# Optimization experiments

Measured on AMD Instinct MI355X. Metric: run time of the kernel, lower is better.

Reference implementation:

```python
import jax, jax.numpy as jnp
import numpy as np

C = 256
NUM_HEADS = 4
GROUPS = 8
EPS = 1e-5


def setup_inputs() -> dict:
    key = jax.random.key(0)
    ks = jax.random.split(key, 7)
    B, H, W = 4, 64, 64
    x = jax.random.normal(ks[0], (B, C, H, W), dtype=jnp.float32)
    # GroupNorm affine params
    norm_w = jnp.ones((C,), dtype=jnp.float32)
    norm_b = jnp.zeros((C,), dtype=jnp.float32)
    # 1x1 convs == channel-mixing matrices
    qkv_w = jax.random.normal(ks[1], (3 * C, C), dtype=jnp.float32) * (C ** -0.5)
    qkv_b = jnp.zeros((3 * C,), dtype=jnp.float32)
    proj_w = jax.random.normal(ks[2], (C, C), dtype=jnp.float32) * (C ** -0.5)
    proj_b = jnp.zeros((C,), dtype=jnp.float32)
    return {"x": x, "norm_w": norm_w, "norm_b": norm_b,
            "qkv_w": qkv_w, "qkv_b": qkv_b,
            "proj_w": proj_w, "proj_b": proj_b}


def _group_norm(x, w, b):
    B, Cc, H, W = x.shape
    xr = x.reshape(B, GROUPS, Cc // GROUPS, H * W)
    mean = xr.mean(axis=(2, 3), keepdims=True)
    var = xr.var(axis=(2, 3), keepdims=True)
    xn = ((xr - mean) * jax.lax.rsqrt(var + EPS)).reshape(B, Cc, H, W)
    return xn * w[None, :, None, None] + b[None, :, None, None]


def reference(x, norm_w, norm_b, qkv_w, qkv_b, proj_w, proj_b):
    B, Cc, H, W = x.shape
    nh = NUM_HEADS
    d = Cc // nh
    h = _group_norm(x, norm_w, norm_b)
    # 1x1 conv: channel matmul
    qkv = jnp.einsum('oc,bchw->bohw', qkv_w, h) + qkv_b[None, :, None, None]
    q, k, v = jnp.split(qkv, 3, axis=1)
    q = q.reshape(B, nh, d, H * W)
    k = k.reshape(B, nh, d, H * W)
    v = v.reshape(B, nh, d, H * W)
    scale = d ** -0.5
    attn = jnp.einsum('bhci,bhcj->bhij', q, k) * scale  # [B, nh, HW, HW]
    attn = jax.nn.softmax(attn, axis=-1)
    o = jnp.einsum('bhij,bhcj->bhci', attn, v).reshape(B, Cc, H, W)
    out = jnp.einsum('oc,bchw->bohw', proj_w, o) + proj_b[None, :, None, None]
    return x + out
```

## Files before the change

kernel.cpp:

```cpp
#include <hip/hip_runtime.h>

typedef unsigned short u16;
typedef __attribute__((ext_vector_type(8))) short bf16x8;
typedef __attribute__((ext_vector_type(16))) float f32x16;
typedef __attribute__((ext_vector_type(2))) int i32x2;

#define MFMA32(A, B, C) __builtin_amdgcn_mfma_f32_32x32x16_bf16((A), (B), (C), 0, 0, 0)

#define BB 4
#define CC 256
#define HW 4096
#define NH 4
#define HD 64

#define QSCALE 0.18033688f

__device__ __forceinline__ u16 f2bf(float f) {
  unsigned int u = __builtin_bit_cast(unsigned int, f);
  u += 0x7fffu + ((u >> 16) & 1u);
  return (u16)(u >> 16);
}

__device__ __forceinline__ unsigned cvtpk(float a, float b) {
  unsigned r;
  asm("v_cvt_pk_bf16_f32 %0, %1, %2" : "=v"(r) : "v"(a), "v"(b));
  return r;
}

__device__ __forceinline__ uint4 pack_oct(const f32x16& a, int oct, float scl) {
  const int b8 = oct * 8;
  unsigned A0 = cvtpk(a[b8 + 0] * scl, a[b8 + 1] * scl);
  unsigned A1 = cvtpk(a[b8 + 2] * scl, a[b8 + 3] * scl);
  unsigned B0 = cvtpk(a[b8 + 4] * scl, a[b8 + 5] * scl);
  unsigned B1 = cvtpk(a[b8 + 6] * scl, a[b8 + 7] * scl);
  i32x2 r0 = __builtin_amdgcn_permlane32_swap((int)A0, (int)B0, false, false);
  i32x2 r1 = __builtin_amdgcn_permlane32_swap((int)A1, (int)B1, false, false);
  union { unsigned w[4]; uint4 v; } u;
  u.w[0] = (unsigned)r0[0]; u.w[1] = (unsigned)r1[0];
  u.w[2] = (unsigned)r0[1]; u.w[3] = (unsigned)r1[1];
  return u.v;
}

__global__ __launch_bounds__(256) void w2bf_kernel(const float* __restrict__ qw,
                                                   const float* __restrict__ pw,
                                                   u16* __restrict__ w_f) {
  int wv = (blockIdx.x * 256 + threadIdx.x) >> 6;
  int lane = threadIdx.x & 63;
  int row = (wv >> 4) * 32 + (lane & 31);
  int c0 = (wv & 15) * 16 + (lane >> 5) * 8;
  const float* src = (row < 768) ? (qw + (size_t)row * 256 + c0)
                                 : (pw + (size_t)(row - 768) * 256 + c0);
  float4 a = *(const float4*)src;
  float4 b = *(const float4*)(src + 4);
  union { u16 u[8]; uint4 v; } pk;
  pk.u[0] = f2bf(a.x); pk.u[1] = f2bf(a.y); pk.u[2] = f2bf(a.z); pk.u[3] = f2bf(a.w);
  pk.u[4] = f2bf(b.x); pk.u[5] = f2bf(b.y); pk.u[6] = f2bf(b.z); pk.u[7] = f2bf(b.w);
  *(uint4*)(w_f + ((size_t)wv * 64 + lane) * 8) = pk.v;
}

__global__ __launch_bounds__(256) void gn_partial_kernel(const float* __restrict__ x,
                                                         float* __restrict__ partial) {
  const float4* p = (const float4*)(x + (size_t)blockIdx.x * 16384);
  float s = 0.f, ss = 0.f;
  for (int i = threadIdx.x; i < 4096; i += 256) {
    float4 v = p[i];
    s += (v.x + v.y) + (v.z + v.w);
    ss += (v.x * v.x + v.y * v.y) + (v.z * v.z + v.w * v.w);
  }
#pragma unroll
  for (int msk = 32; msk; msk >>= 1) {
    s += __shfl_xor(s, msk);
    ss += __shfl_xor(ss, msk);
  }
  __shared__ float red[2][4];
  int wave = threadIdx.x >> 6;
  if ((threadIdx.x & 63) == 0) { red[0][wave] = s; red[1][wave] = ss; }
  __syncthreads();
  if (threadIdx.x == 0) {
    partial[blockIdx.x] = red[0][0] + red[0][1] + red[0][2] + red[0][3];
    partial[256 + blockIdx.x] = red[1][0] + red[1][1] + red[1][2] + red[1][3];
  }
}

__global__ __launch_bounds__(64) void gn_final_kernel(const float* __restrict__ partial,
                                                      float* __restrict__ stats) {
  int bg = threadIdx.x;
  if (bg < 32) {
    float S = 0.f, SS = 0.f;
#pragma unroll
    for (int sp = 0; sp < 8; ++sp) {
      S += partial[bg * 8 + sp];
      SS += partial[256 + bg * 8 + sp];
    }
    const float invN = 1.0f / 131072.0f;
    float mean = S * invN;
    float var = SS * invN - mean * mean;
    stats[bg] = mean;
    stats[32 + bg] = rsqrtf(var + 1e-5f);
  }
}

__global__ __launch_bounds__(256) void norm_t_kernel(const float* __restrict__ x,
                                                     const float* __restrict__ nw,
                                                     const float* __restrict__ nb,
                                                     const float* __restrict__ stats,
                                                     u16* __restrict__ h_f) {
  __shared__ u16 L[256][66];
  int b = blockIdx.y;
  int s0 = blockIdx.x * 64;
  int lane = threadIdx.x & 63, w = threadIdx.x >> 6;
  int c_off = lane >> 4;
  int s_off = (lane & 15) * 4;
  const float* xb = x + (size_t)b * CC * HW;
#pragma unroll 4
  for (int cc = 0; cc < 16; ++cc) {
    int c = w * 64 + cc * 4 + c_off;
    int g = c >> 5;
    float mean = stats[b * 8 + g];
    float rstd = stats[32 + b * 8 + g];
    float a = nw[c] * rstd;
    float b2 = nb[c] - mean * a;
    float4 v = *(const float4*)(xb + (size_t)c * HW + s0 + s_off);
    union { u16 u[4]; uint2 q; } pk;
    pk.u[0] = f2bf(v.x * a + b2);
    pk.u[1] = f2bf(v.y * a + b2);
    pk.u[2] = f2bf(v.z * a + b2);
    pk.u[3] = f2bf(v.w * a + b2);
    *(uint2*)&L[c][s_off] = pk.q;
  }
  __syncthreads();
  u16* hb = h_f + (size_t)b * HW * CC;
  int ql = lane & 31, hi = lane >> 5;
  for (int t = w; t < 32; t += 4) {
    int s32t = t >> 4, kc = t & 15;
    int c0 = kc * 16 + hi * 8;
    int s = s32t * 32 + ql;
    union { u16 u[8]; uint4 v; } pk;
#pragma unroll
    for (int j = 0; j < 8; ++j) pk.u[j] = L[c0 + j][s];
    int s32g = (s0 >> 5) + s32t;
    *(uint4*)(hb + ((size_t)(s32g * 16 + kc) * 64 + lane) * 8) = pk.v;
  }
}

__global__ __launch_bounds__(256) void qkv_kernel(const u16* __restrict__ h_f,
                                                  const u16* __restrict__ w_f,
                                                  const float* __restrict__ qb,
                                                  u16* __restrict__ q_f,
                                                  u16* __restrict__ k_f,
                                                  u16* __restrict__ v_f) {
  int b = blockIdx.z;
  int y = blockIdx.y;
  int lane = threadIdx.x & 63, wave = threadIdx.x >> 6;
  int ql = lane & 31, hi = lane >> 5;
  int s0w = blockIdx.x * 128 + (wave >> 1) * 64;
  int o0w = y * 128 + (wave & 1) * 64;
  bool isV = (y >= 4);
  const u16* hb = h_f + (size_t)b * HW * CC;

  f32x16 acc[2][2];
  if (!isV) {
#pragma unroll
    for (int mo = 0; mo < 2; ++mo)
#pragma unroll
      for (int r = 0; r < 16; ++r) {
        int row = (r & 3) + 8 * (r >> 2) + 4 * hi;
        float bv = qb[o0w + mo * 32 + row];
        acc[mo][0][r] = bv;
        acc[mo][1][r] = bv;
      }
  } else {
#pragma unroll
    for (int ns = 0; ns < 2; ++ns) {
      float bv = qb[o0w + ns * 32 + ql];
#pragma unroll
      for (int r = 0; r < 16; ++r) {
        acc[0][ns][r] = bv;
        acc[1][ns][r] = bv;
      }
    }
  }

  int os32 = o0w >> 5, ss32 = s0w >> 5;
  const u16* wp = w_f + ((size_t)(os32 * 16) * 64 + lane) * 8;
  const u16* hp = hb + ((size_t)(ss32 * 16) * 64 + lane) * 8;
  bf16x8 wf[2], hf[2], wn[2], hn[2];
  wf[0] = *(const bf16x8*)(wp);
  wf[1] = *(const bf16x8*)(wp + 16 * 512);
  hf[0] = *(const bf16x8*)(hp);
  hf[1] = *(const bf16x8*)(hp + 16 * 512);
#pragma unroll 1
  for (int kk = 0; kk < 16; ++kk) {
    if (kk < 15) {
      wn[0] = *(const bf16x8*)(wp + (size_t)(kk + 1) * 512);
      wn[1] = *(const bf16x8*)(wp + (size_t)(16 + kk + 1) * 512);
      hn[0] = *(const bf16x8*)(hp + (size_t)(kk + 1) * 512);
      hn[1] = *(const bf16x8*)(hp + (size_t)(16 + kk + 1) * 512);
    }
    if (!isV) {
      acc[0][0] = MFMA32(wf[0], hf[0], acc[0][0]);
      acc[0][1] = MFMA32(wf[0], hf[1], acc[0][1]);
      acc[1][0] = MFMA32(wf[1], hf[0], acc[1][0]);
      acc[1][1] = MFMA32(wf[1], hf[1], acc[1][1]);
    } else {
      acc[0][0] = MFMA32(hf[0], wf[0], acc[0][0]);
      acc[0][1] = MFMA32(hf[0], wf[1], acc[0][1]);
      acc[1][0] = MFMA32(hf[1], wf[0], acc[1][0]);
      acc[1][1] = MFMA32(hf[1], wf[1], acc[1][1]);
    }
    wf[0] = wn[0]; wf[1] = wn[1]; hf[0] = hn[0]; hf[1] = hn[1];
  }

  if (!isV) {
    bool isQ = (y < 2);
    float scl = isQ ? QSCALE : 1.0f;
    int headL = (o0w >> 6) - (isQ ? 0 : 4);
    u16* base = (isQ ? q_f : k_f) + (size_t)(b * NH + headL) * HW * HD;
#pragma unroll
    for (int mo = 0; mo < 2; ++mo)
#pragma unroll
      for (int ns = 0; ns < 2; ++ns) {
        int s32 = ss32 + ns;
#pragma unroll
        for (int oct = 0; oct < 2; ++oct) {
          int kc = mo * 2 + oct;
          uint4 v = pack_oct(acc[mo][ns], oct, scl);
          *(uint4*)(base + ((size_t)(s32 * 4 + kc) * 64 + lane) * 8) = v;
        }
      }
  } else {
    int headv = (o0w >> 6) - 8;
    u16* base = v_f + (size_t)(b * NH + headv) * HW * HD;
#pragma unroll
    for (int mo = 0; mo < 2; ++mo)
#pragma unroll
      for (int ns = 0; ns < 2; ++ns)
#pragma unroll
        for (int oct = 0; oct < 2; ++oct) {
          int kvb = s0w + mo * 32 + oct * 16;
          int jb64 = kvb >> 6, kcv = (kvb & 63) >> 4;
          uint4 v = pack_oct(acc[mo][ns], oct, 1.0f);
          *(uint4*)(base + ((size_t)((jb64 * 2 + ns) * 4 + kcv) * 64 + lane) * 8) = v;
        }
  }
}

__global__ __launch_bounds__(512) void attn_kernel(const u16* __restrict__ q_f,
                                                   const u16* __restrict__ k_f,
                                                   const u16* __restrict__ v_f,
                                                   u16* __restrict__ o_f) {
  __shared__ float mbuf[4 * 33 * 64];
  int wgid = blockIdx.x + gridDim.x * blockIdx.y;
  int xcd = wgid & 7;
  int j = wgid >> 3;
  int bh = (xcd << 1) | (j & 1);
  int qblk = j >> 1;
  int tid = threadIdx.x;
  int wave = tid >> 6, lane = tid & 63;
  int half = wave >> 2, wsub = wave & 3;
  int ql = lane & 31, hi = lane >> 5;
  int q0w = qblk * 128 + wsub * 32;
  const u16* qfb = q_f + (size_t)bh * HW * HD + lane * 8;
  const u16* kfb = k_f + (size_t)bh * HW * HD + lane * 8;
  const u16* vfb = v_f + (size_t)bh * HW * HD + lane * 8;

  int s32q = q0w >> 5;
  bf16x8 qf[4];
#pragma unroll
  for (int kc = 0; kc < 4; ++kc)
    qf[kc] = *(const bf16x8*)(qfb + (size_t)(s32q * 4 + kc) * 512);

  float l_run = 0.f;
  f32x16 of0 = {}, of1 = {};
  bf16x8 kfr[8], vfr[8];

  {
    const u16* kb = kfb + (size_t)half * 4096;
    const u16* vb = vfb + (size_t)half * 4096;
#pragma unroll
    for (int kc = 0; kc < 4; ++kc) {
      kfr[kc] = *(const bf16x8*)(kb + (size_t)kc * 512);
      kfr[4 + kc] = *(const bf16x8*)(kb + (size_t)(4 + kc) * 512);
      vfr[kc] = *(const bf16x8*)(vb + (size_t)kc * 512);
      vfr[4 + kc] = *(const bf16x8*)(vb + (size_t)(4 + kc) * 512);
    }
  }

#pragma unroll 1
  for (int it = half; it < 64; it += 2) {
    f32x16 s0 = {}, s1 = {};
    __builtin_amdgcn_s_setprio(1);
#pragma unroll
    for (int kc = 0; kc < 4; ++kc) {
      s0 = MFMA32(kfr[kc], qf[kc], s0);
      s1 = MFMA32(kfr[4 + kc], qf[kc], s1);
    }
    __builtin_amdgcn_s_setprio(0);

    {
      const u16* kb = kfb + (size_t)(it + 2) * 4096;
#pragma unroll
      for (int kc = 0; kc < 4; ++kc) {
        kfr[kc] = *(const bf16x8*)(kb + (size_t)kc * 512);
        kfr[4 + kc] = *(const bf16x8*)(kb + (size_t)(4 + kc) * 512);
      }
    }

#pragma unroll
    for (int i = 0; i < 16; ++i) {
      s0[i] = __builtin_amdgcn_exp2f(s0[i]);
      s1[i] = __builtin_amdgcn_exp2f(s1[i]);
    }

    bf16x8 pf[4];
#pragma unroll
    for (int kc = 0; kc < 4; ++kc) {
      const f32x16 pv = (kc < 2) ? s0 : s1;
      const int b8 = (kc & 1) * 8;
      unsigned A0 = cvtpk(pv[b8 + 0], pv[b8 + 1]);
      unsigned A1 = cvtpk(pv[b8 + 2], pv[b8 + 3]);
      unsigned B0 = cvtpk(pv[b8 + 4], pv[b8 + 5]);
      unsigned B1 = cvtpk(pv[b8 + 6], pv[b8 + 7]);
      i32x2 r0 = __builtin_amdgcn_permlane32_swap((int)A0, (int)B0, false, false);
      i32x2 r1 = __builtin_amdgcn_permlane32_swap((int)A1, (int)B1, false, false);
      union { unsigned w[4]; bf16x8 v8; } u;
      u.w[0] = (unsigned)r0[0]; u.w[1] = (unsigned)r1[0];
      u.w[2] = (unsigned)r0[1]; u.w[3] = (unsigned)r1[1];
      pf[kc] = u.v8;
    }

    __builtin_amdgcn_s_setprio(1);
#pragma unroll
    for (int kc = 0; kc < 4; ++kc) {
      of0 = MFMA32(vfr[kc], pf[kc], of0);
      of1 = MFMA32(vfr[4 + kc], pf[kc], of1);
    }
    __builtin_amdgcn_s_setprio(0);

    {
      const u16* vb = vfb + (size_t)(it + 2) * 4096;
#pragma unroll
      for (int kc = 0; kc < 4; ++kc) {
        vfr[kc] = *(const bf16x8*)(vb + (size_t)kc * 512);
        vfr[4 + kc] = *(const bf16x8*)(vb + (size_t)(4 + kc) * 512);
      }
    }

    float t8[8];
#pragma unroll
    for (int i = 0; i < 8; ++i)
      t8[i] = (s0[i] + s0[i + 8]) + (s1[i] + s1[i + 8]);
    float t4a = t8[0] + t8[4], t4b = t8[1] + t8[5];
    float t4c = t8[2] + t8[6], t4d = t8[3] + t8[7];
    l_run += (t4a + t4b) + (t4c + t4d);
  }

  __syncthreads();
  if (half == 1) {
    float* mb = mbuf + (size_t)wsub * 33 * 64 + lane;
#pragma unroll
    for (int i = 0; i < 16; ++i) mb[i * 64] = of0[i];
#pragma unroll
    for (int i = 0; i < 16; ++i) mb[(16 + i) * 64] = of1[i];
    mb[32 * 64] = l_run;
  }
  __syncthreads();
  if (half == 0) {
    const float* mb = mbuf + (size_t)wsub * 33 * 64 + lane;
#pragma unroll
    for (int i = 0; i < 16; ++i) of0[i] += mb[i * 64];
#pragma unroll
    for (int i = 0; i < 16; ++i) of1[i] += mb[(16 + i) * 64];
    l_run += mb[32 * 64];
    float l_tot = l_run + __shfl_xor(l_run, 32);
    float inv_l = 1.0f / l_tot;
    int bb = bh >> 2, hh = bh & 3;
    u16* obase = o_f + (size_t)bb * HW * CC;
    int q32 = q0w >> 5;
#pragma unroll
    for (int cb = 0; cb < 2; ++cb) {
      const f32x16 o = cb ? of1 : of0;
#pragma unroll
      for (int oct = 0; oct < 2; ++oct) {
        int ck = hh * 4 + cb * 2 + oct;
        uint4 v = pack_oct(o, oct, inv_l);
        *(uint4*)(obase + ((size_t)(q32 * 16 + ck) * 64 + lane) * 8) = v;
      }
    }
  }
}

__global__ __launch_bounds__(256) void proj_kernel(const u16* __restrict__ o_f,
                                                   const u16* __restrict__ w_f,
                                                   const float* __restrict__ pb,
                                                   const float* __restrict__ x,
                                                   float* __restrict__ out) {
  int b = blockIdx.z;
  int lane = threadIdx.x & 63, wave = threadIdx.x >> 6;
  int ql = lane & 31, hi = lane >> 5;
  int s0w = blockIdx.x * 128 + (wave >> 1) * 64;
  int o0w = blockIdx.y * 128 + (wave & 1) * 64;
  const u16* ob = o_f + (size_t)b * HW * CC;

  f32x16 acc[2][2];
#pragma unroll
  for (int mo = 0; mo < 2; ++mo)
#pragma unroll
    for (int r = 0; r < 16; ++r) {
      int row = (r & 3) + 8 * (r >> 2) + 4 * hi;
      float bv = pb[o0w + mo * 32 + row];
      acc[mo][0][r] = bv;
      acc[mo][1][r] = bv;
    }

  int os32 = 24 + (o0w >> 5), ss32 = s0w >> 5;
  const u16* wp = w_f + ((size_t)(os32 * 16) * 64 + lane) * 8;
  const u16* op2 = ob + ((size_t)(ss32 * 16) * 64 + lane) * 8;
  bf16x8 af[2], bf2[2], an[2], bn[2];
  af[0] = *(const bf16x8*)(wp);
  af[1] = *(const bf16x8*)(wp + 16 * 512);
  bf2[0] = *(const bf16x8*)(op2);
  bf2[1] = *(const bf16x8*)(op2 + 16 * 512);
#pragma unroll 1
  for (int kk = 0; kk < 16; ++kk) {
    if (kk < 15) {
      an[0] = *(const bf16x8*)(wp + (size_t)(kk + 1) * 512);
      an[1] = *(const bf16x8*)(wp + (size_t)(16 + kk + 1) * 512);
      bn[0] = *(const bf16x8*)(op2 + (size_t)(kk + 1) * 512);
      bn[1] = *(const bf16x8*)(op2 + (size_t)(16 + kk + 1) * 512);
    }
    acc[0][0] = MFMA32(af[0], bf2[0], acc[0][0]);
    acc[0][1] = MFMA32(af[0], bf2[1], acc[0][1]);
    acc[1][0] = MFMA32(af[1], bf2[0], acc[1][0]);
    acc[1][1] = MFMA32(af[1], bf2[1], acc[1][1]);
    af[0] = an[0]; af[1] = an[1]; bf2[0] = bn[0]; bf2[1] = bn[1];
  }

#pragma unroll
  for (int mo = 0; mo < 2; ++mo)
#pragma unroll
    for (int r = 0; r < 16; ++r) {
      int o = o0w + mo * 32 + (r & 3) + 8 * (r >> 2) + 4 * hi;
      const float* xp = x + ((size_t)b * CC + o) * HW + s0w + ql;
      float* op = out + ((size_t)b * CC + o) * HW + s0w + ql;
      op[0] = acc[mo][0][r] + xp[0];
      op[32] = acc[mo][1][r] + xp[32];
    }
}

extern "C" void kernel_launch(void* const* d_in, const int* in_sizes, int n_in,
                              void* d_out, int out_size, void* d_ws, size_t ws_size,
                              hipStream_t stream) {
  const float* x = (const float*)d_in[0];
  const float* nw = (const float*)d_in[1];
  const float* nb = (const float*)d_in[2];
  const float* qw = (const float*)d_in[3];
  const float* qb = (const float*)d_in[4];
  const float* pw = (const float*)d_in[5];
  const float* pb = (const float*)d_in[6];
  float* out = (float*)d_out;

  float* stats = (float*)d_ws;
  float* partial = stats + 64;
  u16* h_f = (u16*)((char*)d_ws + 4096);
  u16* q_f = h_f + (size_t)BB * HW * CC;
  u16* k_f = q_f + (size_t)BB * HW * CC;
  u16* v_f = k_f + (size_t)BB * HW * CC;
  u16* w_f = v_f + (size_t)BB * HW * CC;
  u16* o_f = h_f;

  gn_partial_kernel<<<256, 256, 0, stream>>>(x, partial);
  gn_final_kernel<<<1, 64, 0, stream>>>(partial, stats);
  w2bf_kernel<<<128, 256, 0, stream>>>(qw, pw, w_f);
  norm_t_kernel<<<dim3(HW / 64, BB), 256, 0, stream>>>(x, nw, nb, stats, h_f);
  qkv_kernel<<<dim3(HW / 128, 6, BB), 256, 0, stream>>>(h_f, w_f, qb, q_f, k_f, v_f);
  attn_kernel<<<dim3(HW / 128, BB * NH), 512, 0, stream>>>(q_f, k_f, v_f, o_f);
  proj_kernel<<<dim3(HW / 128, 2, BB), 256, 0, stream>>>(o_f, w_f, pb, x, out);
}
```

Before: 138.1 us.

## Stage h tile in LDS and loop all six output blocks per workgroup in qkv

The qkv kernel now loads the 128-position activation tile once into shared memory and loops over all six 128-row output-channel blocks inside one workgroup, instead of launching one workgroup per output block. This removes the sixfold re-read of h from global memory. In exchange the grid shrinks sixfold (128 workgroups), the register double-buffering prefetch of weights is dropped, and weight loads now sit directly before the MFMAs with no overlap.

```diff
diff --git a/kernel.cpp b/kernel.cpp
--- a/kernel.cpp
+++ b/kernel.cpp
@@ -149,99 +149,106 @@
                                                   u16* __restrict__ q_f,
                                                   u16* __restrict__ k_f,
                                                   u16* __restrict__ v_f) {
-  int b = blockIdx.z;
-  int y = blockIdx.y;
+  __shared__ __align__(16) u16 hL[4][16][64 * 8];
+  int b = blockIdx.y;
   int lane = threadIdx.x & 63, wave = threadIdx.x >> 6;
   int ql = lane & 31, hi = lane >> 5;
-  int s0w = blockIdx.x * 128 + (wave >> 1) * 64;
-  int o0w = y * 128 + (wave & 1) * 64;
-  bool isV = (y >= 4);
+  int s0 = blockIdx.x * 128;
+  int ss32 = s0 >> 5;
   const u16* hb = h_f + (size_t)b * HW * CC;
 
-  f32x16 acc[2][2];
-  if (!isV) {
-#pragma unroll
-    for (int mo = 0; mo < 2; ++mo)
-#pragma unroll
-      for (int r = 0; r < 16; ++r) {
-        int row = (r & 3) + 8 * (r >> 2) + 4 * hi;
-        float bv = qb[o0w + mo * 32 + row];
-        acc[mo][0][r] = bv;
-        acc[mo][1][r] = bv;
-      }
-  } else {
-#pragma unroll
-    for (int ns = 0; ns < 2; ++ns) {
-      float bv = qb[o0w + ns * 32 + ql];
-#pragma unroll
-      for (int r = 0; r < 16; ++r) {
-        acc[0][ns][r] = bv;
-        acc[1][ns][r] = bv;
-      }
-    }
-  }
-
-  int os32 = o0w >> 5, ss32 = s0w >> 5;
-  const u16* wp = w_f + ((size_t)(os32 * 16) * 64 + lane) * 8;
-  const u16* hp = hb + ((size_t)(ss32 * 16) * 64 + lane) * 8;
-  bf16x8 wf[2], hf[2], wn[2], hn[2];
-  wf[0] = *(const bf16x8*)(wp);
-  wf[1] = *(const bf16x8*)(wp + 16 * 512);
-  hf[0] = *(const bf16x8*)(hp);
-  hf[1] = *(const bf16x8*)(hp + 16 * 512);
+  {
+    const u16* src = hb + ((size_t)((ss32 + wave) * 16) * 64 + lane) * 8;
+#pragma unroll
+    for (int kc = 0; kc < 16; ++kc)
+      *(uint4*)&hL[wave][kc][lane * 8] = *(const uint4*)(src + (size_t)kc * 512);
+  }
+  __syncthreads();
+
+  int sw = wave >> 1;
+  int ow = wave & 1;
 #pragma unroll 1
-  for (int kk = 0; kk < 16; ++kk) {
-    if (kk < 15) {
-      wn[0] = *(const bf16x8*)(wp + (size_t)(kk + 1) * 512);
-      wn[1] = *(const bf16x8*)(wp + (size_t)(16 + kk + 1) * 512);
-      hn[0] = *(const bf16x8*)(hp + (size_t)(kk + 1) * 512);
-      hn[1] = *(const bf16x8*)(hp + (size_t)(16 + kk + 1) * 512);
-    }
+  for (int y = 0; y < 6; ++y) {
+    int o0w = y * 128 + ow * 64;
+    bool isV = (y >= 4);
+    f32x16 acc[2][2];
     if (!isV) {
-      acc[0][0] = MFMA32(wf[0], hf[0], acc[0][0]);
-      acc[0][1] = MFMA32(wf[0], hf[1], acc[0][1]);
-      acc[1][0] = MFMA32(wf[1], hf[0], acc[1][0]);
-      acc[1][1] = MFMA32(wf[1], hf[1], acc[1][1]);
+#pragma unroll
+      for (int mo = 0; mo < 2; ++mo)
+#pragma unroll
+        for (int r = 0; r < 16; ++r) {
+          int row = (r & 3) + 8 * (r >> 2) + 4 * hi;
+          float bv = qb[o0w + mo * 32 + row];
+          acc[mo][0][r] = bv;
+          acc[mo][1][r] = bv;
+        }
     } else {
-      acc[0][0] = MFMA32(hf[0], wf[0], acc[0][0]);
-      acc[0][1] = MFMA32(hf[0], wf[1], acc[0][1]);
-      acc[1][0] = MFMA32(hf[1], wf[0], acc[1][0]);
-      acc[1][1] = MFMA32(hf[1], wf[1], acc[1][1]);
-    }
-    wf[0] = wn[0]; wf[1] = wn[1]; hf[0] = hn[0]; hf[1] = hn[1];
-  }
-
-  if (!isV) {
-    bool isQ = (y < 2);
-    float scl = isQ ? QSCALE : 1.0f;
-    int headL = (o0w >> 6) - (isQ ? 0 : 4);
-    u16* base = (isQ ? q_f : k_f) + (size_t)(b * NH + headL) * HW * HD;
-#pragma unroll
-    for (int mo = 0; mo < 2; ++mo)
 #pragma unroll
       for (int ns = 0; ns < 2; ++ns) {
-        int s32 = ss32 + ns;
-#pragma unroll
-        for (int oct = 0; oct < 2; ++oct) {
-          int kc = mo * 2 + oct;
-          uint4 v = pack_oct(acc[mo][ns], oct, scl);
-          *(uint4*)(base + ((size_t)(s32 * 4 + kc) * 64 + lane) * 8) = v;
+        float bv = qb[o0w + ns * 32 + ql];
+#pragma unroll
+        for (int r = 0; r < 16; ++r) {
+          acc[0][ns][r] = bv;
+          acc[1][ns][r] = bv;
         }
       }
-  } else {
-    int headv = (o0w >> 6) - 8;
-    u16* base = v_f + (size_t)(b * NH + headv) * HW * HD;
-#pragma unroll
-    for (int mo = 0; mo < 2; ++mo)
-#pragma unroll
-      for (int ns = 0; ns < 2; ++ns)
-#pragma unroll
-        for (int oct = 0; oct < 2; ++oct) {
-          int kvb = s0w + mo * 32 + oct * 16;
-          int jb64 = kvb >> 6, kcv = (kvb & 63) >> 4;
-          uint4 v = pack_oct(acc[mo][ns], oct, 1.0f);
-          *(uint4*)(base + ((size_t)((jb64 * 2 + ns) * 4 + kcv) * 64 + lane) * 8) = v;
+    }
+
+    int os32 = o0w >> 5;
+    const u16* wp = w_f + ((size_t)(os32 * 16) * 64 + lane) * 8;
+#pragma unroll 1
+    for (int kk = 0; kk < 16; ++kk) {
+      bf16x8 wf[2], hf[2];
+      wf[0] = *(const bf16x8*)(wp + (size_t)kk * 512);
+      wf[1] = *(const bf16x8*)(wp + (size_t)(16 + kk) * 512);
+      hf[0] = *(const bf16x8*)&hL[sw * 2 + 0][kk][lane * 8];
+      hf[1] = *(const bf16x8*)&hL[sw * 2 + 1][kk][lane * 8];
+      if (!isV) {
+        acc[0][0] = MFMA32(wf[0], hf[0], acc[0][0]);
+        acc[0][1] = MFMA32(wf[0], hf[1], acc[0][1]);
+        acc[1][0] = MFMA32(wf[1], hf[0], acc[1][0]);
+        acc[1][1] = MFMA32(wf[1], hf[1], acc[1][1]);
+      } else {
+        acc[0][0] = MFMA32(hf[0], wf[0], acc[0][0]);
+        acc[0][1] = MFMA32(hf[0], wf[1], acc[0][1]);
+        acc[1][0] = MFMA32(hf[1], wf[0], acc[1][0]);
+        acc[1][1] = MFMA32(hf[1], wf[1], acc[1][1]);
+      }
+    }
+
+    int sbase = ss32 + sw * 2;
+    if (!isV) {
+      bool isQ = (y < 2);
+      float scl = isQ ? QSCALE : 1.0f;
+      int headL = (o0w >> 6) - (isQ ? 0 : 4);
+      u16* base = (isQ ? q_f : k_f) + (size_t)(b * NH + headL) * HW * HD;
+#pragma unroll
+      for (int mo = 0; mo < 2; ++mo)
+#pragma unroll
+        for (int ns = 0; ns < 2; ++ns) {
+          int s32 = sbase + ns;
+#pragma unroll
+          for (int oct = 0; oct < 2; ++oct) {
+            int kc = mo * 2 + oct;
+            uint4 v = pack_oct(acc[mo][ns], oct, scl);
+            *(uint4*)(base + ((size_t)(s32 * 4 + kc) * 64 + lane) * 8) = v;
+          }
         }
+    } else {
+      int headv = (o0w >> 6) - 8;
+      u16* base = v_f + (size_t)(b * NH + headv) * HW * HD;
+#pragma unroll
+      for (int mo = 0; mo < 2; ++mo)
+#pragma unroll
+        for (int ns = 0; ns < 2; ++ns)
+#pragma unroll
+          for (int oct = 0; oct < 2; ++oct) {
+            int kvb = sbase * 32 + mo * 32 + oct * 16;
+            int jb64 = kvb >> 6, kcv = (kvb & 63) >> 4;
+            uint4 v = pack_oct(acc[mo][ns], oct, 1.0f);
+            *(uint4*)(base + ((size_t)((jb64 * 2 + ns) * 4 + kcv) * 64 + lane) * 8) = v;
+          }
+    }
   }
 }
 
@@ -473,7 +480,7 @@
   gn_final_kernel<<<1, 64, 0, stream>>>(partial, stats);
   w2bf_kernel<<<128, 256, 0, stream>>>(qw, pw, w_f);
   norm_t_kernel<<<dim3(HW / 64, BB), 256, 0, stream>>>(x, nw, nb, stats, h_f);
-  qkv_kernel<<<dim3(HW / 128, 6, BB), 256, 0, stream>>>(h_f, w_f, qb, q_f, k_f, v_f);
+  qkv_kernel<<<dim3(HW / 128, BB), 256, 0, stream>>>(h_f, w_f, qb, q_f, k_f, v_f);
   attn_kernel<<<dim3(HW / 128, BB * NH), 512, 0, stream>>>(q_f, k_f, v_f, o_f);
   proj_kernel<<<dim3(HW / 128, 2, BB), 256, 0, stream>>>(o_f, w_f, pb, x, out);
 }
```

Measured after the change: 169.7 us. +22.9%, slower.
